# Kernel tuning notes

Hardware: AMD Instinct MI355X
Metric: run time of the kernel (lower is better)

## Reference

```python
import jax, jax.numpy as jnp
import numpy as np

V, H, L, NH, DH, FF, P, T = 21128, 768, 12, 12, 64, 3072, 512, 9
B, S = 16, 256
EPS = 1e-12

def _ln(x, g, b):
    m = x.mean(-1, keepdims=True)
    v = ((x - m) ** 2).mean(-1, keepdims=True)
    return (x - m) * jax.lax.rsqrt(v + EPS) * g + b

def setup_inputs() -> dict:
    key = jax.random.key(0)
    ks = iter(jax.random.split(key, 64))
    def nrm(shape, s=0.02):
        return (jax.random.normal(next(ks), shape, jnp.float32) * s)
    inp = {
        'input_ids': jax.random.randint(next(ks), (B, 1, S), 0, V, dtype=jnp.int32),
        'token_type_ids': jnp.zeros((B, 1, S), jnp.int32),
        'attention_mask': jnp.ones((B, 1, S), jnp.int32),
        'tags': jax.random.randint(next(ks), (B, S), 0, T, dtype=jnp.int32),
        'word_emb': nrm((V, H)), 'pos_emb': nrm((P, H)), 'type_emb': nrm((2, H)),
        'emb_ln_g': jnp.ones((H,), jnp.float32), 'emb_ln_b': jnp.zeros((H,), jnp.float32),
        'Wq': nrm((L, H, H)), 'bq': jnp.zeros((L, H), jnp.float32),
        'Wk': nrm((L, H, H)), 'bk': jnp.zeros((L, H), jnp.float32),
        'Wv': nrm((L, H, H)), 'bv': jnp.zeros((L, H), jnp.float32),
        'Wo': nrm((L, H, H)), 'bo': jnp.zeros((L, H), jnp.float32),
        'ln1_g': jnp.ones((L, H), jnp.float32), 'ln1_b': jnp.zeros((L, H), jnp.float32),
        'W1': nrm((L, H, FF)), 'b1': jnp.zeros((L, FF), jnp.float32),
        'W2': nrm((L, FF, H)), 'b2': jnp.zeros((L, H), jnp.float32),
        'ln2_g': jnp.ones((L, H), jnp.float32), 'ln2_b': jnp.zeros((L, H), jnp.float32),
        'dense_W': nrm((H, T)), 'dense_b': jnp.zeros((T,), jnp.float32),
        'crf_start': nrm((T,), 0.1), 'crf_end': nrm((T,), 0.1), 'crf_trans': nrm((T, T), 0.1),
    }
    return inp

def _model(input_ids, token_type_ids, attention_mask, tags,
           word_emb, pos_emb, type_emb, emb_ln_g, emb_ln_b,
           Wq, bq, Wk, bk, Wv, bv, Wo, bo, ln1_g, ln1_b,
           W1, b1, W2, b2, ln2_g, ln2_b, dense_W, dense_b,
           crf_start, crf_end, crf_trans):
    ids = input_ids[:, 0, :]            # [B,S]
    tt = token_type_ids[:, 0, :]
    amask = attention_mask[:, 0, :]     # [B,S] int
    Bn, Sn = ids.shape
    # --- BERT embeddings (post-LN BERT-base) ---
    x = word_emb[ids] + pos_emb[:Sn][None, :, :] + type_emb[tt]
    x = _ln(x, emb_ln_g, emb_ln_b)
    bias = jnp.where(amask[:, None, None, :] > 0, 0.0, -1e9).astype(x.dtype)  # [B,1,1,S]
    scale = 1.0 / np.sqrt(DH).astype(np.float32)
    def layer(h, p):
        wq, bq_, wk, bk_, wv, bv_, wo, bo_, g1, c1, w1, d1, w2, d2, g2, c2 = p
        q = (h @ wq + bq_).reshape(Bn, Sn, NH, DH).transpose(0, 2, 1, 3)
        k = (h @ wk + bk_).reshape(Bn, Sn, NH, DH).transpose(0, 2, 1, 3)
        v = (h @ wv + bv_).reshape(Bn, Sn, NH, DH).transpose(0, 2, 1, 3)
        att = jax.nn.softmax(jnp.einsum('bhqd,bhkd->bhqk', q, k) * scale + bias, axis=-1)
        ctx = jnp.einsum('bhqk,bhkd->bhqd', att, v).transpose(0, 2, 1, 3).reshape(Bn, Sn, H)
        h = _ln(h + ctx @ wo + bo_, g1, c1)
        ff = jax.nn.gelu(h @ w1 + d1, approximate=False)
        h = _ln(h + ff @ w2 + d2, g2, c2)
        return h, None
    x, _ = jax.lax.scan(layer, x, (Wq, bq, Wk, bk, Wv, bv, Wo, bo, ln1_g, ln1_b, W1, b1, W2, b2, ln2_g, ln2_b))
    # --- emission head, seq-first like the torch code ---
    emis = (x @ dense_W + dense_b).transpose(1, 0, 2)   # [S,B,T]
    m = (amask.T > 0)                                    # [S,B] bool
    tags_sb = tags.T                                     # [S,B]
    bidx = jnp.arange(Bn)
    # --- CRF numerator (gold path score) ---
    score0 = crf_start[tags_sb[0]] + emis[0, bidx, tags_sb[0]]
    def num_step(sc, inp):
        e, t, tp, mm = inp
        inc = crf_trans[tp, t] + e[bidx, t]
        return sc + jnp.where(mm, inc, 0.0), None
    score, _ = jax.lax.scan(num_step, score0, (emis[1:], tags_sb[1:], tags_sb[:-1], m[1:]))
    lengths = m.astype(jnp.int32).sum(0)                 # [B]
    last_tag = jnp.take_along_axis(tags_sb, (lengths - 1)[None, :], axis=0)[0]
    score = score + crf_end[last_tag]
    # --- CRF partition (forward algorithm) ---
    alpha0 = crf_start[None, :] + emis[0]                # [B,T]
    def fwd_step(a, inp):
        e, mm = inp
        nxt = jax.nn.logsumexp(a[:, :, None] + crf_trans[None, :, :] + e[:, None, :], axis=1)
        return jnp.where(mm[:, None], nxt, a), None
    alpha, _ = jax.lax.scan(fwd_step, alpha0, (emis[1:], m[1:]))
    logZ = jax.nn.logsumexp(alpha + crf_end[None, :], axis=-1)
    loss = -(score - logZ).mean()                        # reduction='mean'
    # --- Viterbi decode ---
    v0 = crf_start[None, :] + emis[0]
    tid = jnp.arange(T)
    def vit_step(vv, inp):
        e, mm = inp
        sc = vv[:, :, None] + crf_trans[None, :, :]       # [B,T,T]
        nv = sc.max(1) + e
        idx = sc.argmax(1).astype(jnp.int32)
        vv2 = jnp.where(mm[:, None], nv, vv)
        idx = jnp.where(mm[:, None], idx, tid[None, :].astype(jnp.int32))
        return vv2, idx
    vfin, hist = jax.lax.scan(vit_step, v0, (emis[1:], m[1:]))  # hist: [S-1,B,T]
    last = jnp.argmax(vfin + crf_end[None, :], axis=-1).astype(jnp.int32)  # [B]
    def back_step(t, h):
        prev = jnp.take_along_axis(h, t[:, None], axis=1)[:, 0]
        return prev, prev
    _, path = jax.lax.scan(back_step, last, hist, reverse=True)  # [S-1,B]
    preds = jnp.concatenate([path, last[None, :]], axis=0).T     # [B,S]
    return loss, preds

def reference(input_ids, token_type_ids, attention_mask, tags,
              word_emb, pos_emb, type_emb, emb_ln_g, emb_ln_b,
              Wq, bq, Wk, bk, Wv, bv, Wo, bo, ln1_g, ln1_b,
              W1, b1, W2, b2, ln2_g, ln2_b, dense_W, dense_b,
              crf_start, crf_end, crf_trans):
    return _model(input_ids, token_type_ids, attention_mask, tags,
                  word_emb, pos_emb, type_emb, emb_ln_g, emb_ln_b,
                  Wq, bq, Wk, bk, Wv, bv, Wo, bo, ln1_g, ln1_b,
                  W1, b1, W2, b2, ln2_g, ln2_b, dense_W, dense_b,
                  crf_start, crf_end, crf_trans)
```

## Files before the change

### kernel.cpp

```cpp
#include <hip/hip_runtime.h>
#include <math.h>

#define B_ 16
#define S_ 256
#define H_ 768
#define L_ 12
#define NH_ 12
#define DH_ 64
#define FF_ 3072
#define T_ 9

typedef unsigned short ushort_t;
typedef __attribute__((ext_vector_type(8))) __bf16 bf16x8;
typedef __attribute__((ext_vector_type(4))) float f32x4;
typedef __attribute__((ext_vector_type(4))) unsigned short us4;
typedef __attribute__((ext_vector_type(4))) unsigned int u32x4;

__device__ __forceinline__ ushort_t f2bf(float f) {
  union { float f; unsigned u; } v; v.f = f;
  unsigned r = v.u + 0x7FFFu + ((v.u >> 16) & 1u);
  return (ushort_t)(r >> 16);
}
__device__ __forceinline__ float bf2f(ushort_t h) {
  union { unsigned u; float f; } v; v.u = ((unsigned)h) << 16;
  return v.f;
}
__device__ __forceinline__ void gload16(const void* g, void* l) {
  __builtin_amdgcn_global_load_lds((const __attribute__((address_space(1))) void*)g,
                                   (__attribute__((address_space(3))) void*)l, 16, 0, 0);
}

__global__ __launch_bounds__(256) void emb_ln_kernel(const int* __restrict__ ids, const int* __restrict__ tt,
                              const float* __restrict__ we, const float* __restrict__ pe,
                              const float* __restrict__ te, const float* __restrict__ g,
                              const float* __restrict__ bb, float* __restrict__ out,
                              ushort_t* __restrict__ oh, ushort_t* __restrict__ ol) {
  const int token = blockIdx.x;
  const int tid = threadIdx.x;
  const int s = token & (S_ - 1);
  const int id = ids[token];
  const int t2 = tt[token];
  float x[3];
  float sum = 0.f;
#pragma unroll
  for (int i = 0; i < 3; ++i) {
    int d = tid + i * 256;
    x[i] = we[(size_t)id * H_ + d] + pe[(size_t)s * H_ + d] + te[(size_t)t2 * H_ + d];
    sum += x[i];
  }
  __shared__ float red[4];
#pragma unroll
  for (int o = 32; o > 0; o >>= 1) sum += __shfl_xor(sum, o, 64);
  const int wid = tid >> 6, lane = tid & 63;
  if (lane == 0) red[wid] = sum;
  __syncthreads();
  const float mean = (red[0] + red[1] + red[2] + red[3]) * (1.f / H_);
  float vs = 0.f;
#pragma unroll
  for (int i = 0; i < 3; ++i) { float dv = x[i] - mean; vs += dv * dv; }
#pragma unroll
  for (int o = 32; o > 0; o >>= 1) vs += __shfl_xor(vs, o, 64);
  __syncthreads();
  if (lane == 0) red[wid] = vs;
  __syncthreads();
  const float var = (red[0] + red[1] + red[2] + red[3]) * (1.f / H_);
  const float inv = rsqrtf(var + 1e-12f);
  float* op = out + (size_t)token * H_;
  ushort_t* hp = oh + (size_t)token * H_;
  ushort_t* lp = ol + (size_t)token * H_;
#pragma unroll
  for (int i = 0; i < 3; ++i) {
    int d = tid + i * 256;
    float y = (x[i] - mean) * inv * g[d] + bb[d];
    op[d] = y;
    ushort_t h = f2bf(y);
    hp[d] = h;
    lp[d] = f2bf(y - bf2f(h));
  }
}

__global__ __launch_bounds__(256) void ln_kernel(const float* __restrict__ base, const float* __restrict__ delta,
                          const float* __restrict__ g, const float* __restrict__ bb,
                          float* __restrict__ out, ushort_t* __restrict__ oh, ushort_t* __restrict__ ol) {
  const int token = blockIdx.x;
  const int tid = threadIdx.x;
  const float* bp = base + (size_t)token * H_;
  const float* dp = delta + (size_t)token * H_;
  float x[3];
  float s = 0.f;
#pragma unroll
  for (int i = 0; i < 3; ++i) { int d = tid + i * 256; x[i] = bp[d] + dp[d]; s += x[i]; }
  __shared__ float red[4];
#pragma unroll
  for (int o = 32; o > 0; o >>= 1) s += __shfl_xor(s, o, 64);
  const int wid = tid >> 6, lane = tid & 63;
  if (lane == 0) red[wid] = s;
  __syncthreads();
  const float mean = (red[0] + red[1] + red[2] + red[3]) * (1.f / H_);
  float vs = 0.f;
#pragma unroll
  for (int i = 0; i < 3; ++i) { float dv = x[i] - mean; vs += dv * dv; }
#pragma unroll
  for (int o = 32; o > 0; o >>= 1) vs += __shfl_xor(vs, o, 64);
  __syncthreads();
  if (lane == 0) red[wid] = vs;
  __syncthreads();
  const float var = (red[0] + red[1] + red[2] + red[3]) * (1.f / H_);
  const float inv = rsqrtf(var + 1e-12f);
  float* op = out + (size_t)token * H_;
  ushort_t* hp = oh + (size_t)token * H_;
  ushort_t* lp = ol + (size_t)token * H_;
#pragma unroll
  for (int i = 0; i < 3; ++i) {
    int d = tid + i * 256;
    float y = (x[i] - mean) * inv * g[d] + bb[d];
    op[d] = y;
    ushort_t h = f2bf(y);
    hp[d] = h;
    lp[d] = f2bf(y - bf2f(h));
  }
}

__device__ __forceinline__ void transpose_core(float (*t)[65], const float* __restrict__ src,
                                               ushort_t* __restrict__ dh,
                                               int K, int N, int n0, int k0) {
  const int tid = threadIdx.x;
#pragma unroll
  for (int i = 0; i < 16; ++i) {
    int lin = tid + i * 256;
    int kk = lin >> 6, nn = lin & 63;
    t[kk][nn] = src[(size_t)(k0 + kk) * N + n0 + nn];
  }
  __syncthreads();
#pragma unroll
  for (int i = 0; i < 16; ++i) {
    int lin = tid + i * 256;
    int nn = lin >> 6, kk = lin & 63;
    dh[(size_t)(n0 + nn) * K + k0 + kk] = f2bf(t[kk][nn]);
  }
}

__device__ __forceinline__ void wprep_dispatch(float (*t)[65], int wid,
                        const float* Wq, const float* Wk, const float* Wv, const float* Wo,
                        const float* W1, const float* W2,
                        ushort_t* WT4h, ushort_t* W1th, ushort_t* W2th) {
  if (wid < 576) {
    const int z = wid / 144, r = wid - z * 144;
    const int x = r % 12, y = r / 12;
    const float* src = z == 0 ? Wq : (z == 1 ? Wk : (z == 2 ? Wv : Wo));
    transpose_core(t, src, WT4h + (size_t)z * H_ * H_, H_, H_, x * 64, y * 64);
  } else if (wid < 1152) {
    const int i = wid - 576;
    const int x = i % 48, y = i / 48;
    transpose_core(t, W1, W1th, H_, FF_, x * 64, y * 64);
  } else {
    const int i = wid - 1152;
    const int x = i % 12, y = i / 12;
    transpose_core(t, W2, W2th, FF_, H_, x * 64, y * 64);
  }
}

__global__ __launch_bounds__(256) void wprep_k(const float* __restrict__ Wq, const float* __restrict__ Wk,
                        const float* __restrict__ Wv, const float* __restrict__ Wo,
                        const float* __restrict__ W1, const float* __restrict__ W2,
                        ushort_t* __restrict__ WT4h,
                        ushort_t* __restrict__ W1th, ushort_t* __restrict__ W2th) {
  __shared__ float t[64][65];
  wprep_dispatch(t, blockIdx.x, Wq, Wk, Wv, Wo, W1, W2, WT4h, W1th, W2th);
}

template <int R>
__device__ __forceinline__ void stage_slice(const ushort_t* __restrict__ gsrc, int K, char* lds) {
  const int tid = threadIdx.x;
  constexpr int NIT = (R * 4) / 256;
#pragma unroll
  for (int i = 0; i < NIT; ++i) {
    const int v = tid + i * 256;
    const int kh = v / (2 * R);
    const int r2 = v & (2 * R - 1);
    const int row = r2 >> 1;
    const int kg = (kh << 1) | ((r2 & 1) ^ ((row >> 2) & 1));
    gload16(gsrc + (size_t)row * K + kg * 8, lds + (i * 256 + (tid & 192)) * 16);
  }
}

template <int BM, int BN, int BK>
__device__ __forceinline__ void mgemm_acc(
    const ushort_t* __restrict__ Ah, const ushort_t* __restrict__ Al,
    const ushort_t* __restrict__ Bth,
    int K, f32x4 (&acc)[BM / 32][BN / 32], char* pool) {
  constexpr int FM = BM / 32;
  constexpr int FN = BN / 32;
  constexpr int ABYTES = BM * BK * 2;
  constexpr int BBYTES = BN * BK * 2;
  constexpr int BUF = 2 * ABYTES + BBYTES;
  const int tid = threadIdx.x;
  const int w = tid >> 6, lane = tid & 63;
  const int wm = w >> 1, wn = w & 1;
  const int kgL = lane >> 4, lr = lane & 15;
  const int row0 = blockIdx.y * BM, col0 = blockIdx.x * BN;

#pragma unroll
  for (int i = 0; i < FM; ++i)
#pragma unroll
    for (int j = 0; j < FN; ++j) acc[i][j] = (f32x4){0.f, 0.f, 0.f, 0.f};

  const int khL = kgL >> 1;
  const int swz = (((kgL & 1) ^ ((lr >> 2) & 1)) << 4);
  const int aB0 = khL * (BM * 32) + (wm * (BM / 2) + lr) * 32 + swz;
  const int bB0 = khL * (BN * 32) + (wn * (BN / 2) + lr) * 32 + swz;

  const ushort_t* gA_h = Ah + (size_t)row0 * K;
  const ushort_t* gA_l = Al + (size_t)row0 * K;
  const ushort_t* gB_h = Bth + (size_t)col0 * K;

  auto stageall = [&](int k0, char* buf) {
#pragma unroll
    for (int c = 0; c < BK / 32; ++c) {
      stage_slice<BM>(gA_h + k0 + c * 32, K, buf + c * BM * 64);
      stage_slice<BM>(gA_l + k0 + c * 32, K, buf + ABYTES + c * BM * 64);
      stage_slice<BN>(gB_h + k0 + c * 32, K, buf + 2 * ABYTES + c * BN * 64);
    }
  };

  const int nk = K / BK;
  stageall(0, pool);
  for (int k = 0; k < nk; ++k) {
    char* cur = pool + (k & 1) * BUF;
    if (k + 1 < nk) {
      stageall((k + 1) * BK, pool + ((k + 1) & 1) * BUF);
      asm volatile("s_waitcnt vmcnt(6)" ::: "memory");
    } else {
      asm volatile("s_waitcnt vmcnt(0)" ::: "memory");
    }
    __builtin_amdgcn_s_barrier();
    asm volatile("" ::: "memory");

#pragma unroll
    for (int ks = 0; ks < BK / 32; ++ks) {
      const char* aP = cur + ks * BM * 64;
      const char* bP = cur + 2 * ABYTES + ks * BN * 64;
      bf16x8 a_h[FM], a_l[FM], b_h[FN];
#pragma unroll
      for (int fm = 0; fm < FM; ++fm) {
        a_h[fm] = *(const bf16x8*)(aP + aB0 + fm * 512);
        a_l[fm] = *(const bf16x8*)(aP + ABYTES + aB0 + fm * 512);
      }
#pragma unroll
      for (int fn = 0; fn < FN; ++fn) {
        b_h[fn] = *(const bf16x8*)(bP + bB0 + fn * 512);
      }
#pragma unroll
      for (int fm = 0; fm < FM; ++fm)
#pragma unroll
        for (int fn = 0; fn < FN; ++fn) {
          f32x4 c = acc[fm][fn];
          c = __builtin_amdgcn_mfma_f32_16x16x32_bf16(a_h[fm], b_h[fn], c, 0, 0, 0);
          c = __builtin_amdgcn_mfma_f32_16x16x32_bf16(a_l[fm], b_h[fn], c, 0, 0, 0);
          acc[fm][fn] = c;
        }
    }
    asm volatile("" ::: "memory");
    __builtin_amdgcn_s_barrier();
  }
}

template <int BM, int BN, int BK, int EPI>
__global__ __launch_bounds__(256, 3) void mgemm(const ushort_t* __restrict__ Ah, const ushort_t* __restrict__ Al,
                      const ushort_t* __restrict__ Bth,
                      const float* __restrict__ bias, float* __restrict__ Cf,
                      ushort_t* __restrict__ Ch, ushort_t* __restrict__ Cl, int N, int K) {
  __shared__ __attribute__((aligned(16))) char pool[2 * (2 * BM * BK + BN * BK) * 2];
  f32x4 acc[BM / 32][BN / 32];
  mgemm_acc<BM, BN, BK>(Ah, Al, Bth, K, acc, pool);
  const int tid = threadIdx.x;
  const int w = tid >> 6, lane = tid & 63;
  const int wm = w >> 1, wn = w & 1;
  const int kg = lane >> 4, lr = lane & 15;
  const int row0 = blockIdx.y * BM, col0 = blockIdx.x * BN;
#pragma unroll
  for (int fn = 0; fn < BN / 32; ++fn) {
    const int col = col0 + wn * (BN / 2) + fn * 16 + lr;
    const float bv = bias[col];
#pragma unroll
    for (int fm = 0; fm < BM / 32; ++fm) {
#pragma unroll
      for (int r = 0; r < 4; ++r) {
        const int row = row0 + wm * (BM / 2) + fm * 16 + kg * 4 + r;
        float v = acc[fm][fn][r] + bv;
        if (EPI == 0) {
          Cf[(size_t)row * N + col] = v;
        } else {
          float gl = 0.5f * v * (1.f + erff(v * 0.70710678118654752f));
          ushort_t h = f2bf(gl);
          Ch[(size_t)row * N + col] = h;
          Cl[(size_t)row * N + col] = f2bf(gl - bf2f(h));
        }
      }
    }
  }
}

__global__ __launch_bounds__(256, 3) void ff1_fused(
    const ushort_t* __restrict__ Xh, const ushort_t* __restrict__ Xl,
    const ushort_t* __restrict__ W1th, const float* __restrict__ bias,
    ushort_t* __restrict__ Ch, ushort_t* __restrict__ Cl,
    const float* __restrict__ WqN, const float* __restrict__ WkN,
    const float* __restrict__ WvN, const float* __restrict__ WoN,
    const float* __restrict__ W1N, const float* __restrict__ W2N,
    ushort_t* __restrict__ WT4hN, ushort_t* __restrict__ W1thN, ushort_t* __restrict__ W2thN) {
  __shared__ __attribute__((aligned(16))) char pool[49152];
  if (blockIdx.y >= 32) {
    if (WqN == nullptr) return;
    const int wid = (blockIdx.y - 32) * 24 + blockIdx.x;
    wprep_dispatch((float(*)[65])pool, wid, WqN, WkN, WvN, WoN, W1N, W2N, WT4hN, W1thN, W2thN);
    return;
  }
  f32x4 acc[4][4];
  mgemm_acc<128, 128, 32>(Xh, Xl, W1th, H_, acc, pool);
  const int tid = threadIdx.x;
  const int w = tid >> 6, lane = tid & 63;
  const int wm = w >> 1, wn = w & 1;
  const int kg = lane >> 4, lr = lane & 15;
  const int row0 = blockIdx.y * 128, col0 = blockIdx.x * 128;
#pragma unroll
  for (int fn = 0; fn < 4; ++fn) {
    const int col = col0 + wn * 64 + fn * 16 + lr;
    const float bv = bias[col];
#pragma unroll
    for (int fm = 0; fm < 4; ++fm) {
#pragma unroll
      for (int r = 0; r < 4; ++r) {
        const int row = row0 + wm * 64 + fm * 16 + kg * 4 + r;
        float v = acc[fm][fn][r] + bv;
        float gl = 0.5f * v * (1.f + erff(v * 0.70710678118654752f));
        ushort_t h = f2bf(gl);
        Ch[(size_t)row * FF_ + col] = h;
        Cl[(size_t)row * FF_ + col] = f2bf(gl - bf2f(h));
      }
    }
  }
}

__global__ __launch_bounds__(256) void qkv_m(const ushort_t* __restrict__ Xh, const ushort_t* __restrict__ Xl,
                      const ushort_t* __restrict__ WT4h,
                      const float* __restrict__ bq, const float* __restrict__ bk,
                      const float* __restrict__ bvv,
                      ushort_t* __restrict__ Qh, ushort_t* __restrict__ Ql,
                      ushort_t* __restrict__ Kh, ushort_t* __restrict__ Vth) {
  constexpr int ABYTES = 128 * 32 * 2;
  constexpr int BUF = 2 * ABYTES + 3 * ABYTES;
  __shared__ __attribute__((aligned(16))) char pool[2 * BUF];
  const int tid = threadIdx.x;
  const int w = tid >> 6, lane = tid & 63;
  const int wm = w >> 1, wn = w & 1;
  const int kgL = lane >> 4, lr = lane & 15;
  const int row0 = blockIdx.y * 128, col0 = blockIdx.x * 128;

  f32x4 acc[3][4][4];
#pragma unroll
  for (int z = 0; z < 3; ++z)
#pragma unroll
    for (int i = 0; i < 4; ++i)
#pragma unroll
      for (int j = 0; j < 4; ++j) acc[z][i][j] = (f32x4){0.f, 0.f, 0.f, 0.f};

  const int khL = kgL >> 1;
  const int swz = (((kgL & 1) ^ ((lr >> 2) & 1)) << 4);
  const int aB0 = khL * (128 * 32) + (wm * 64 + lr) * 32 + swz;
  const int bB0 = khL * (128 * 32) + (wn * 64 + lr) * 32 + swz;

  const ushort_t* gA_h = Xh + (size_t)row0 * H_;
  const ushort_t* gA_l = Xl + (size_t)row0 * H_;
  const ushort_t* gB0 = WT4h + (size_t)col0 * H_;
  const ushort_t* gB1 = WT4h + (size_t)H_ * H_ + (size_t)col0 * H_;
  const ushort_t* gB2 = WT4h + (size_t)2 * H_ * H_ + (size_t)col0 * H_;

  auto stageall = [&](int k0, char* buf) {
    stage_slice<128>(gA_h + k0, H_, buf);
    stage_slice<128>(gA_l + k0, H_, buf + ABYTES);
    stage_slice<128>(gB0 + k0, H_, buf + 2 * ABYTES);
    stage_slice<128>(gB1 + k0, H_, buf + 3 * ABYTES);
    stage_slice<128>(gB2 + k0, H_, buf + 4 * ABYTES);
  };

  const int nk = H_ / 32;
  stageall(0, pool);
  for (int k = 0; k < nk; ++k) {
    char* cur = pool + (k & 1) * BUF;
    if (k + 1 < nk) {
      stageall((k + 1) * 32, pool + ((k + 1) & 1) * BUF);
      asm volatile("s_waitcnt vmcnt(10)" ::: "memory");
    } else {
      asm volatile("s_waitcnt vmcnt(0)" ::: "memory");
    }
    __builtin_amdgcn_s_barrier();
    asm volatile("" ::: "memory");

    bf16x8 a_h[4], a_l[4];
#pragma unroll
    for (int fm = 0; fm < 4; ++fm) {
      a_h[fm] = *(const bf16x8*)(cur + aB0 + fm * 512);
      a_l[fm] = *(const bf16x8*)(cur + ABYTES + aB0 + fm * 512);
    }
#pragma unroll
    for (int z = 0; z < 3; ++z) {
      const char* bP = cur + (2 + z) * ABYTES;
      bf16x8 b_h[4];
#pragma unroll
      for (int fn = 0; fn < 4; ++fn) b_h[fn] = *(const bf16x8*)(bP + bB0 + fn * 512);
#pragma unroll
      for (int fm = 0; fm < 4; ++fm)
#pragma unroll
        for (int fn = 0; fn < 4; ++fn) {
          f32x4 c = acc[z][fm][fn];
          c = __builtin_amdgcn_mfma_f32_16x16x32_bf16(a_h[fm], b_h[fn], c, 0, 0, 0);
          c = __builtin_amdgcn_mfma_f32_16x16x32_bf16(a_l[fm], b_h[fn], c, 0, 0, 0);
          acc[z][fm][fn] = c;
        }
    }
    asm volatile("" ::: "memory");
    __builtin_amdgcn_s_barrier();
  }

  const int kg = kgL;
#pragma unroll
  for (int fn = 0; fn < 4; ++fn) {
    const int col = col0 + wn * 64 + fn * 16 + lr;
    const float bvq = bq[col], bvk = bk[col], bvv2 = bvv[col];
#pragma unroll
    for (int fm = 0; fm < 4; ++fm) {
      const int rowb = row0 + wm * 64 + fm * 16 + kg * 4;
#pragma unroll
      for (int r = 0; r < 4; ++r) {
        float v = acc[0][fm][fn][r] + bvq;
        ushort_t h = f2bf(v);
        Qh[(size_t)(rowb + r) * H_ + col] = h;
        Ql[(size_t)(rowb + r) * H_ + col] = f2bf(v - bf2f(h));
      }
#pragma unroll
      for (int r = 0; r < 4; ++r) {
        Kh[(size_t)(rowb + r) * H_ + col] = f2bf(acc[1][fm][fn][r] + bvk);
      }
      {
        us4 h4;
#pragma unroll
        for (int r = 0; r < 4; ++r) h4[r] = f2bf(acc[2][fm][fn][r] + bvv2);
        const int bb2 = rowb >> 8, s0 = rowb & 255;
        const int hh2 = col >> 6, d = col & 63;
        *(us4*)(Vth + ((size_t)(bb2 * NH_ + hh2) * DH_ + d) * S_ + s0) = h4;
      }
    }
  }
}

__global__ __launch_bounds__(256, 3) void attn_mfma(
    const ushort_t* __restrict__ Qh, const ushort_t* __restrict__ Ql,
    const ushort_t* __restrict__ Kh, const ushort_t* __restrict__ Vth,
    const int* __restrict__ amask,
    ushort_t* __restrict__ Oh, ushort_t* __restrict__ Ol) {
  const int bid = blockIdx.x;
  const int qt = bid / 192;
  const int gh = bid - qt * 192;
  const int b = gh / NH_;
  const int h = gh - b * NH_;
  __shared__ __attribute__((aligned(16))) ushort_t sKh[2][64 * 64];
  __shared__ __attribute__((aligned(16))) ushort_t sVh[2][64 * 64];
  __shared__ __attribute__((aligned(16))) unsigned sP[4][16 * 68];
  __shared__ float sBias[2][64];
  const int tid = threadIdx.x;
  const int w = tid >> 6, lane = tid & 63;
  const int kg = lane >> 4, lr = lane & 15;

  const int qrow = b * S_ + qt * 64 + w * 16 + lr;
  bf16x8 qfh[2], qfl[2];
#pragma unroll
  for (int ds2 = 0; ds2 < 2; ++ds2) {
    const size_t off = (size_t)qrow * H_ + h * DH_ + ds2 * 32 + kg * 8;
    qfh[ds2] = *(const bf16x8*)(Qh + off);
    qfl[ds2] = *(const bf16x8*)(Ql + off);
  }

  f32x4 ctx[4];
#pragma unroll
  for (int i = 0; i < 4; ++i) ctx[i] = (f32x4){0.f, 0.f, 0.f, 0.f};
  float mrow[4], lrw[4];
#pragma unroll
  for (int r = 0; r < 4; ++r) { mrow[r] = -1e30f; lrw[r] = 0.f; }

  unsigned* sPw = &sP[w][0];

  auto stageKV = [&](int kt, int bufi) {
#pragma unroll
    for (int i = 0; i < 2; ++i) {
      const int v = tid + i * 256;
      const int row = v >> 3;
      const int c16 = (v & 7) ^ (row & 7);
      const size_t kgl = (size_t)(b * S_ + kt * 64 + row) * H_ + h * DH_ + c16 * 8;
      gload16(Kh + kgl, (char*)&sKh[bufi][0] + v * 16);
      const size_t vgl = (size_t)((b * NH_ + h) * DH_ + row) * S_ + kt * 64 + c16 * 8;
      gload16(Vth + vgl, (char*)&sVh[bufi][0] + v * 16);
    }
    if (tid < 64) sBias[bufi][tid] = (amask[b * S_ + kt * 64 + tid] > 0) ? 0.f : -1e9f;
  };

  stageKV(0, 0);
  for (int kt = 0; kt < 4; ++kt) {
    const int bi = kt & 1;
    if (kt < 3) {
      stageKV(kt + 1, bi ^ 1);
      asm volatile("s_waitcnt vmcnt(4) lgkmcnt(0)" ::: "memory");
    } else {
      asm volatile("s_waitcnt vmcnt(0) lgkmcnt(0)" ::: "memory");
    }
    __builtin_amdgcn_s_barrier();
    asm volatile("" ::: "memory");

    f32x4 sc[4];
#pragma unroll
    for (int kf = 0; kf < 4; ++kf) sc[kf] = (f32x4){0.f, 0.f, 0.f, 0.f};
#pragma unroll
    for (int kf = 0; kf < 4; ++kf) {
      const int krow = kf * 16 + lr;
#pragma unroll
      for (int ds2 = 0; ds2 < 2; ++ds2) {
        const int cb = (ds2 * 64 + kg * 16) ^ ((krow & 7) << 4);
        const bf16x8 kvh = *(const bf16x8*)((const char*)&sKh[bi][0] + krow * 128 + cb);
        sc[kf] = __builtin_amdgcn_mfma_f32_16x16x32_bf16(qfh[ds2], kvh, sc[kf], 0, 0, 0);
        sc[kf] = __builtin_amdgcn_mfma_f32_16x16x32_bf16(qfl[ds2], kvh, sc[kf], 0, 0, 0);
      }
    }
    float bsv[4];
#pragma unroll
    for (int kf = 0; kf < 4; ++kf) bsv[kf] = sBias[bi][kf * 16 + lr];

#pragma unroll
    for (int r = 0; r < 4; ++r) {
      float sv[4];
      float tmax = -1e30f;
#pragma unroll
      for (int kf = 0; kf < 4; ++kf) {
        sv[kf] = sc[kf][r] * 0.125f + bsv[kf];
        tmax = fmaxf(tmax, sv[kf]);
      }
#pragma unroll
      for (int o = 8; o > 0; o >>= 1) tmax = fmaxf(tmax, __shfl_xor(tmax, o, 64));
      const float mnew = fmaxf(mrow[r], tmax);
      const float corr = expf(mrow[r] - mnew);
      float ls = 0.f;
      const int qoff = (kg * 4 + r) * 68;
#pragma unroll
      for (int kf = 0; kf < 4; ++kf) {
        const float pe = expf(sv[kf] - mnew);
        ls += pe;
        const ushort_t hi = f2bf(pe);
        const ushort_t lo = f2bf(pe - bf2f(hi));
        sPw[qoff + kf * 16 + lr] = ((unsigned)hi << 16) | lo;
      }
#pragma unroll
      for (int o = 8; o > 0; o >>= 1) ls += __shfl_xor(ls, o, 64);
      lrw[r] = lrw[r] * corr + ls;
      mrow[r] = mnew;
#pragma unroll
      for (int df = 0; df < 4; ++df) ctx[df][r] *= corr;
    }

#pragma unroll
    for (int ks = 0; ks < 2; ++ks) {
      unsigned w8[8];
      *(u32x4*)&w8[0] = *(const u32x4*)(sPw + lr * 68 + ks * 32 + kg * 8);
      *(u32x4*)&w8[4] = *(const u32x4*)(sPw + lr * 68 + ks * 32 + kg * 8 + 4);
      union { bf16x8 v; ushort_t u[8]; } ph, pl;
#pragma unroll
      for (int j = 0; j < 8; ++j) { ph.u[j] = (ushort_t)(w8[j] >> 16); pl.u[j] = (ushort_t)(w8[j] & 0xffffu); }
#pragma unroll
      for (int df = 0; df < 4; ++df) {
        const int vrow = df * 16 + lr;
        const int cb = (ks * 64 + kg * 16) ^ ((vrow & 7) << 4);
        const bf16x8 vvh = *(const bf16x8*)((const char*)&sVh[bi][0] + vrow * 128 + cb);
        ctx[df] = __builtin_amdgcn_mfma_f32_16x16x32_bf16(ph.v, vvh, ctx[df], 0, 0, 0);
        ctx[df] = __builtin_amdgcn_mfma_f32_16x16x32_bf16(pl.v, vvh, ctx[df], 0, 0, 0);
      }
    }
    asm volatile("" ::: "memory");
    __builtin_amdgcn_s_barrier();
  }

#pragma unroll
  for (int r = 0; r < 4; ++r) {
    const float inv = 1.f / lrw[r];
    const int tok = b * S_ + qt * 64 + w * 16 + kg * 4 + r;
#pragma unroll
    for (int df = 0; df < 4; ++df) {
      const float v = ctx[df][r] * inv;
      const ushort_t hi = f2bf(v);
      const size_t o = (size_t)tok * H_ + h * DH_ + df * 16 + lr;
      Oh[o] = hi;
      Ol[o] = f2bf(v - bf2f(hi));
    }
  }
}

__global__ __launch_bounds__(256) void emis_kernel(const float* __restrict__ X, const float* __restrict__ W,
                            const float* __restrict__ bias, float* __restrict__ E) {
  const int wave = (blockIdx.x * 256 + threadIdx.x) >> 6;
  const int lane = threadIdx.x & 63;
  const int b = wave >> 8, s = wave & 255;
  const float* xp = X + (size_t)wave * H_;
  float acc[T_];
#pragma unroll
  for (int t = 0; t < T_; ++t) acc[t] = 0.f;
  for (int i = 0; i < 12; ++i) {
    const int d = lane + i * 64;
    const float xv = xp[d];
    const float* wp = W + (size_t)d * T_;
#pragma unroll
    for (int t = 0; t < T_; ++t) acc[t] = fmaf(xv, wp[t], acc[t]);
  }
#pragma unroll
  for (int t = 0; t < T_; ++t) {
    float v = acc[t];
#pragma unroll
    for (int o = 32; o > 0; o >>= 1) v += __shfl_xor(v, o, 64);
    acc[t] = v;
  }
  if (lane < T_) E[((size_t)s * B_ + b) * T_ + lane] = acc[lane] + bias[lane];
}

__global__ __launch_bounds__(128) void crf_kernel(const float* __restrict__ emis, const int* __restrict__ tags,
                          const int* __restrict__ amask,
                          const float* __restrict__ crf_start, const float* __restrict__ crf_end,
                          const float* __restrict__ trans,
                          float* __restrict__ partial, float* __restrict__ out) {
  const int b = blockIdx.x;
  const int tid = threadIdx.x;
  const int wv = tid >> 6;
  const int lane = tid & 63;
  __shared__ float sE[S_ * T_];
  __shared__ float sM[S_];
  __shared__ float trs[T_ * T_];
  __shared__ unsigned char hist[S_ - 1][16];
  __shared__ float pathf[S_];
  for (int i = tid; i < S_ * T_; i += 128) {
    const int s = i / T_, t = i - s * T_;
    sE[i] = emis[((size_t)s * B_ + b) * T_ + t];
  }
  for (int i = tid; i < S_; i += 128) sM[i] = (float)amask[b * S_ + i];
  for (int i = tid; i < T_ * T_; i += 128) trs[i] = trans[i];
  __syncthreads();

  const int t = lane;
  const bool act = t < T_;
  float trc[T_];
#pragma unroll
  for (int p = 0; p < T_; ++p) trc[p] = act ? trs[p * T_ + t] : 0.f;

  if (wv == 0) {
    float alpha = act ? crf_start[t] + sE[t] : 0.f;
    for (int s = 1; s < S_; ++s) {
      float ap[T_];
#pragma unroll
      for (int p = 0; p < T_; ++p) ap[p] = __shfl(alpha, p, 64);
      if (act) {
        const float e = sE[s * T_ + t];
        float mx = -1e30f;
#pragma unroll
        for (int p = 0; p < T_; ++p) mx = fmaxf(mx, ap[p] + trc[p]);
        float sum = 0.f;
#pragma unroll
        for (int p = 0; p < T_; ++p) sum += __expf(ap[p] + trc[p] - mx);
        const float na = mx + __logf(sum) + e;
        if (sM[s] > 0.f) alpha = na;
      }
    }
    float nsum = 0.f;
    int len = 0;
#pragma unroll
    for (int j = 0; j < 4; ++j) {
      const int s = lane + j * 64;
      const int mk = (sM[s] > 0.f) ? 1 : 0;
      len += mk;
      if (s >= 1 && mk) {
        const int tc = tags[b * S_ + s], tp = tags[b * S_ + s - 1];
        nsum += trs[tp * T_ + tc] + sE[s * T_ + tc];
      }
    }
#pragma unroll
    for (int o = 32; o > 0; o >>= 1) {
      nsum += __shfl_xor(nsum, o, 64);
      len += __shfl_xor(len, o, 64);
    }
    const float fz = act ? alpha + crf_end[t] : -1e30f;
    float zp[T_];
#pragma unroll
    for (int p = 0; p < T_; ++p) zp[p] = __shfl(fz, p, 64);
    if (lane == 0) {
      float mx = -1e30f;
#pragma unroll
      for (int p = 0; p < T_; ++p) mx = fmaxf(mx, zp[p]);
      float sum = 0.f;
#pragma unroll
      for (int p = 0; p < T_; ++p) sum += __expf(zp[p] - mx);
      const float logZ = mx + __logf(sum);
      const int tg0 = tags[b * S_];
      const float score = nsum + crf_start[tg0] + sE[tg0] + crf_end[tags[b * S_ + len - 1]];
      partial[b] = score - logZ;
    }
  } else {
    float vit = act ? crf_start[t] + sE[t] : 0.f;
    for (int s = 1; s < S_; ++s) {
      float vp[T_];
#pragma unroll
      for (int p = 0; p < T_; ++p) vp[p] = __shfl(vit, p, 64);
      if (act) {
        const float e = sE[s * T_ + t];
        float best = -1e30f; int bi = 0;
#pragma unroll
        for (int p = 0; p < T_; ++p) {
          const float scv = vp[p] + trc[p];
          if (scv > best) { best = scv; bi = p; }
        }
        if (sM[s] > 0.f) {
          vit = best + e;
          hist[s - 1][t] = (unsigned char)bi;
        } else {
          hist[s - 1][t] = (unsigned char)t;
        }
      }
    }
    const float fv = act ? vit + crf_end[t] : -1e30f;
    float wp[T_];
#pragma unroll
    for (int p = 0; p < T_; ++p) wp[p] = __shfl(fv, p, 64);
    if (lane == 0) {
      float best = -1e30f; int lastTag = 0;
#pragma unroll
      for (int p = 0; p < T_; ++p) {
        if (wp[p] > best) { best = wp[p]; lastTag = p; }
      }
      int tc = lastTag;
      pathf[S_ - 1] = (float)tc;
      for (int i = S_ - 2; i >= 0; --i) {
        tc = hist[i][tc];
        pathf[i] = (float)tc;
      }
    }
  }
  __syncthreads();
#pragma unroll
  for (int j = 0; j < 2; ++j) {
    const int s = tid + j * 128;
    out[1 + b * S_ + s] = pathf[s];
  }
}

__global__ __launch_bounds__(64) void crf_final(const float* __restrict__ partial, float* __restrict__ out) {
  const int lane = threadIdx.x;
  float v = (lane < B_) ? partial[lane] : 0.f;
#pragma unroll
  for (int o = 32; o > 0; o >>= 1) v += __shfl_xor(v, o, 64);
  if (lane == 0) out[0] = -(v * (1.f / B_));
}

extern "C" void kernel_launch(void* const* d_in, const int* in_sizes, int n_in,
                              void* d_out, int out_size, void* d_ws, size_t ws_size,
                              hipStream_t stream) {
  const int* input_ids = (const int*)d_in[0];
  const int* token_type_ids = (const int*)d_in[1];
  const int* attention_mask = (const int*)d_in[2];
  const int* tags = (const int*)d_in[3];
  const float* word_emb = (const float*)d_in[4];
  const float* pos_emb = (const float*)d_in[5];
  const float* type_emb = (const float*)d_in[6];
  const float* emb_ln_g = (const float*)d_in[7];
  const float* emb_ln_b = (const float*)d_in[8];
  const float* Wq = (const float*)d_in[9];
  const float* bq = (const float*)d_in[10];
  const float* Wk = (const float*)d_in[11];
  const float* bk = (const float*)d_in[12];
  const float* Wv = (const float*)d_in[13];
  const float* bv = (const float*)d_in[14];
  const float* Wo = (const float*)d_in[15];
  const float* bo = (const float*)d_in[16];
  const float* ln1_g = (const float*)d_in[17];
  const float* ln1_b = (const float*)d_in[18];
  const float* W1 = (const float*)d_in[19];
  const float* b1 = (const float*)d_in[20];
  const float* W2 = (const float*)d_in[21];
  const float* b2 = (const float*)d_in[22];
  const float* ln2_g = (const float*)d_in[23];
  const float* ln2_b = (const float*)d_in[24];
  const float* dense_W = (const float*)d_in[25];
  const float* dense_b = (const float*)d_in[26];
  const float* crf_start = (const float*)d_in[27];
  const float* crf_end = (const float*)d_in[28];
  const float* crf_trans = (const float*)d_in[29];

  constexpr size_t NTOK = (size_t)B_ * S_;
  constexpr size_t XSZ = NTOK * H_;
  constexpr size_t WT4SZ = (size_t)4 * H_ * H_;
  constexpr size_t WFSZ = (size_t)H_ * FF_;

  char* p = (char*)d_ws;
  float* X = (float*)p;            p += XSZ * 4;
  float* TMP = (float*)p;          p += XSZ * 4;
  char* UN = p;                    p += 8 * XSZ * 2;
  ushort_t* Qh = (ushort_t*)UN;
  ushort_t* Ql = Qh + XSZ;
  ushort_t* Kh = Ql + XSZ;
  ushort_t* Vth = Kh + XSZ;
  ushort_t* CTXh = Vth + XSZ;
  ushort_t* CTXl = CTXh + XSZ;
  ushort_t* FFh = (ushort_t*)UN;
  ushort_t* FFl = FFh + NTOK * FF_;
  ushort_t* Xh = (ushort_t*)p;     p += XSZ * 2;
  ushort_t* Xl = (ushort_t*)p;     p += XSZ * 2;
  ushort_t* WT4h2 = (ushort_t*)p;  p += WT4SZ * 2 * 2;
  ushort_t* W1th2 = (ushort_t*)p;  p += WFSZ * 2 * 2;
  ushort_t* W2th2 = (ushort_t*)p;  p += WFSZ * 2 * 2;
  float* EM = (float*)p;           p += (size_t)S_ * B_ * T_ * 4;
  float* PART = (float*)p;         p += B_ * 4;

  emb_ln_kernel<<<dim3(4096), dim3(256), 0, stream>>>(input_ids, token_type_ids, word_emb, pos_emb,
                                                      type_emb, emb_ln_g, emb_ln_b, X, Xh, Xl);
  wprep_k<<<dim3(1728), dim3(256), 0, stream>>>(Wq, Wk, Wv, Wo, W1, W2, WT4h2, W1th2, W2th2);

  for (int l = 0; l < L_; ++l) {
    const int pr = l & 1, pn = (l + 1) & 1;
    ushort_t* WT4h = WT4h2 + (size_t)pr * WT4SZ;
    ushort_t* W1th = W1th2 + (size_t)pr * WFSZ;
    ushort_t* W2th = W2th2 + (size_t)pr * WFSZ;
    const bool hasNext = (l + 1 < L_);
    const size_t wo_n = (size_t)(l + 1) * H_ * H_;

    qkv_m<<<dim3(6, 32), dim3(256), 0, stream>>>(Xh, Xl, WT4h, bq + (size_t)l * H_,
                                                 bk + (size_t)l * H_, bv + (size_t)l * H_,
                                                 Qh, Ql, Kh, Vth);
    attn_mfma<<<dim3(768), dim3(256), 0, stream>>>(Qh, Ql, Kh, Vth, attention_mask, CTXh, CTXl);
    mgemm<128, 128, 32, 0><<<dim3(6, 32), dim3(256), 0, stream>>>(
        CTXh, CTXl, WT4h + (size_t)3 * H_ * H_,
        bo + (size_t)l * H_, TMP, nullptr, nullptr, H_, H_);
    ln_kernel<<<dim3(4096), dim3(256), 0, stream>>>(X, TMP, ln1_g + (size_t)l * H_,
                                                    ln1_b + (size_t)l * H_, X, Xh, Xl);
    ff1_fused<<<dim3(24, 32 + 72), dim3(256), 0, stream>>>(
        Xh, Xl, W1th, b1 + (size_t)l * FF_, FFh, FFl,
        hasNext ? Wq + wo_n : nullptr, Wk + wo_n, Wv + wo_n, Wo + wo_n,
        W1 + (size_t)(l + 1) * WFSZ, W2 + (size_t)(l + 1) * WFSZ,
        WT4h2 + (size_t)pn * WT4SZ, W1th2 + (size_t)pn * WFSZ, W2th2 + (size_t)pn * WFSZ);
    mgemm<128, 128, 32, 0><<<dim3(6, 32), dim3(256), 0, stream>>>(
        FFh, FFl, W2th, b2 + (size_t)l * H_, TMP, nullptr, nullptr, H_, FF_);
    ln_kernel<<<dim3(4096), dim3(256), 0, stream>>>(X, TMP, ln2_g + (size_t)l * H_,
                                                    ln2_b + (size_t)l * H_, X, Xh, Xl);
  }

  emis_kernel<<<dim3(1024), dim3(256), 0, stream>>>(X, dense_W, dense_b, EM);
  crf_kernel<<<dim3(B_), dim3(128), 0, stream>>>(EM, tags, attention_mask, crf_start, crf_end,
                                                 crf_trans, PART, (float*)d_out);
  crf_final<<<dim3(1), dim3(64), 0, stream>>>(PART, (float*)d_out);
}
```

Baseline: 3.163 ms.

## Widen FF1 tile to 128x256, fuse final LN with emissions, LDS broadcast in CRF

The FF1 GEMM now uses 128x256 tiles with a larger LDS pool and lower occupancy (launch bounds 2). The grid is halved in x, the weight-prep block count is doubled to keep the same coverage, and the vmcnt wait is made tile-dependent. The last layer's LayerNorm is fused with the 9-tag emission projection, which drops a kernel launch and a full read of X. The CRF forward and Viterbi loops broadcast per-tag values through LDS instead of nine shuffles. The wider tile gives more reuse but means fewer blocks and more register pressure.

```diff
diff --git a/kernel.cpp b/kernel.cpp
--- a/kernel.cpp
+++ b/kernel.cpp
@@ -118,6 +118,67 @@
     ushort_t h = f2bf(y);
     hp[d] = h;
     lp[d] = f2bf(y - bf2f(h));
+  }
+}
+
+__global__ __launch_bounds__(256) void ln_emis_kernel(const float* __restrict__ base, const float* __restrict__ delta,
+                               const float* __restrict__ g, const float* __restrict__ bb,
+                               const float* __restrict__ W, const float* __restrict__ wbias,
+                               float* __restrict__ E) {
+  const int token = blockIdx.x;
+  const int tid = threadIdx.x;
+  __shared__ float sW[H_ * T_];
+  __shared__ float red[4];
+  __shared__ float wred[4][12];
+  for (int i = tid; i < H_ * T_; i += 256) sW[i] = W[i];
+
+  const float* bp = base + (size_t)token * H_;
+  const float* dp = delta + (size_t)token * H_;
+  float x[3];
+  float s = 0.f;
+#pragma unroll
+  for (int i = 0; i < 3; ++i) { int d = tid + i * 256; x[i] = bp[d] + dp[d]; s += x[i]; }
+#pragma unroll
+  for (int o = 32; o > 0; o >>= 1) s += __shfl_xor(s, o, 64);
+  const int wid = tid >> 6, lane = tid & 63;
+  if (lane == 0) red[wid] = s;
+  __syncthreads();
+  const float mean = (red[0] + red[1] + red[2] + red[3]) * (1.f / H_);
+  float vs = 0.f;
+#pragma unroll
+  for (int i = 0; i < 3; ++i) { float dv = x[i] - mean; vs += dv * dv; }
+#pragma unroll
+  for (int o = 32; o > 0; o >>= 1) vs += __shfl_xor(vs, o, 64);
+  __syncthreads();
+  if (lane == 0) red[wid] = vs;
+  __syncthreads();
+  const float var = (red[0] + red[1] + red[2] + red[3]) * (1.f / H_);
+  const float inv = rsqrtf(var + 1e-12f);
+
+  float acc9[T_];
+#pragma unroll
+  for (int t = 0; t < T_; ++t) acc9[t] = 0.f;
+#pragma unroll
+  for (int i = 0; i < 3; ++i) {
+    int d = tid + i * 256;
+    float y = (x[i] - mean) * inv * g[d] + bb[d];
+    const float* wr = sW + d * T_;
+#pragma unroll
+    for (int t = 0; t < T_; ++t) acc9[t] = fmaf(y, wr[t], acc9[t]);
+  }
+#pragma unroll
+  for (int o = 32; o > 0; o >>= 1)
+#pragma unroll
+    for (int t = 0; t < T_; ++t) acc9[t] += __shfl_xor(acc9[t], o, 64);
+  if (lane == 0) {
+#pragma unroll
+    for (int t = 0; t < T_; ++t) wred[wid][t] = acc9[t];
+  }
+  __syncthreads();
+  if (tid < T_) {
+    const float v = wred[0][tid] + wred[1][tid] + wred[2][tid] + wred[3][tid] + wbias[tid];
+    const int b2 = token >> 8, s2 = token & 255;
+    E[((size_t)s2 * B_ + b2) * T_ + tid] = v;
   }
 }
 
@@ -194,6 +255,7 @@
   constexpr int ABYTES = BM * BK * 2;
   constexpr int BBYTES = BN * BK * 2;
   constexpr int BUF = 2 * ABYTES + BBYTES;
+  constexpr int NL = (8 * BM + 4 * BN) / 256;
   const int tid = threadIdx.x;
   const int w = tid >> 6, lane = tid & 63;
   const int wm = w >> 1, wn = w & 1;
@@ -229,7 +291,13 @@
     char* cur = pool + (k & 1) * BUF;
     if (k + 1 < nk) {
       stageall((k + 1) * BK, pool + ((k + 1) & 1) * BUF);
-      asm volatile("s_waitcnt vmcnt(6)" ::: "memory");
+      if constexpr (NL == 6) {
+        asm volatile("s_waitcnt vmcnt(6)" ::: "memory");
+      } else if constexpr (NL == 8) {
+        asm volatile("s_waitcnt vmcnt(8)" ::: "memory");
+      } else {
+        asm volatile("s_waitcnt vmcnt(0)" ::: "memory");
+      }
     } else {
       asm volatile("s_waitcnt vmcnt(0)" ::: "memory");
     }
@@ -301,7 +369,7 @@
   }
 }
 
-__global__ __launch_bounds__(256, 3) void ff1_fused(
+__global__ __launch_bounds__(256, 2) void ff1_fused(
     const ushort_t* __restrict__ Xh, const ushort_t* __restrict__ Xl,
     const ushort_t* __restrict__ W1th, const float* __restrict__ bias,
     ushort_t* __restrict__ Ch, ushort_t* __restrict__ Cl,
@@ -309,23 +377,23 @@
     const float* __restrict__ WvN, const float* __restrict__ WoN,
     const float* __restrict__ W1N, const float* __restrict__ W2N,
     ushort_t* __restrict__ WT4hN, ushort_t* __restrict__ W1thN, ushort_t* __restrict__ W2thN) {
-  __shared__ __attribute__((aligned(16))) char pool[49152];
+  __shared__ __attribute__((aligned(16))) char pool[2 * (2 * 128 * 32 + 256 * 32) * 2];
   if (blockIdx.y >= 32) {
     if (WqN == nullptr) return;
-    const int wid = (blockIdx.y - 32) * 24 + blockIdx.x;
+    const int wid = (blockIdx.y - 32) * 12 + blockIdx.x;
     wprep_dispatch((float(*)[65])pool, wid, WqN, WkN, WvN, WoN, W1N, W2N, WT4hN, W1thN, W2thN);
     return;
   }
-  f32x4 acc[4][4];
-  mgemm_acc<128, 128, 32>(Xh, Xl, W1th, H_, acc, pool);
+  f32x4 acc[4][8];
+  mgemm_acc<128, 256, 32>(Xh, Xl, W1th, H_, acc, pool);
   const int tid = threadIdx.x;
   const int w = tid >> 6, lane = tid & 63;
   const int wm = w >> 1, wn = w & 1;
   const int kg = lane >> 4, lr = lane & 15;
-  const int row0 = blockIdx.y * 128, col0 = blockIdx.x * 128;
-#pragma unroll
-  for (int fn = 0; fn < 4; ++fn) {
-    const int col = col0 + wn * 64 + fn * 16 + lr;
+  const int row0 = blockIdx.y * 128, col0 = blockIdx.x * 256;
+#pragma unroll
+  for (int fn = 0; fn < 8; ++fn) {
+    const int col = col0 + wn * 128 + fn * 16 + lr;
     const float bv = bias[col];
 #pragma unroll
     for (int fm = 0; fm < 4; ++fm) {
@@ -601,32 +669,6 @@
   }
 }
 
-__global__ __launch_bounds__(256) void emis_kernel(const float* __restrict__ X, const float* __restrict__ W,
-                            const float* __restrict__ bias, float* __restrict__ E) {
-  const int wave = (blockIdx.x * 256 + threadIdx.x) >> 6;
-  const int lane = threadIdx.x & 63;
-  const int b = wave >> 8, s = wave & 255;
-  const float* xp = X + (size_t)wave * H_;
-  float acc[T_];
-#pragma unroll
-  for (int t = 0; t < T_; ++t) acc[t] = 0.f;
-  for (int i = 0; i < 12; ++i) {
-    const int d = lane + i * 64;
-    const float xv = xp[d];
-    const float* wp = W + (size_t)d * T_;
-#pragma unroll
-    for (int t = 0; t < T_; ++t) acc[t] = fmaf(xv, wp[t], acc[t]);
-  }
-#pragma unroll
-  for (int t = 0; t < T_; ++t) {
-    float v = acc[t];
-#pragma unroll
-    for (int o = 32; o > 0; o >>= 1) v += __shfl_xor(v, o, 64);
-    acc[t] = v;
-  }
-  if (lane < T_) E[((size_t)s * B_ + b) * T_ + lane] = acc[lane] + bias[lane];
-}
-
 __global__ __launch_bounds__(128) void crf_kernel(const float* __restrict__ emis, const int* __restrict__ tags,
                           const int* __restrict__ amask,
                           const float* __restrict__ crf_start, const float* __restrict__ crf_end,
@@ -641,6 +683,7 @@
   __shared__ float trs[T_ * T_];
   __shared__ unsigned char hist[S_ - 1][16];
   __shared__ float pathf[S_];
+  __shared__ __attribute__((aligned(16))) float sBr[2][16];
   for (int i = tid; i < S_ * T_; i += 128) {
     const int s = i / T_, t = i - s * T_;
     sE[i] = emis[((size_t)s * B_ + b) * T_ + t];
@@ -658,17 +701,23 @@
   if (wv == 0) {
     float alpha = act ? crf_start[t] + sE[t] : 0.f;
     for (int s = 1; s < S_; ++s) {
-      float ap[T_];
-#pragma unroll
-      for (int p = 0; p < T_; ++p) ap[p] = __shfl(alpha, p, 64);
+      if (act) sBr[0][t] = alpha;
+      asm volatile("s_waitcnt lgkmcnt(0)" ::: "memory");
+      float ap[12];
+      *(f32x4*)&ap[0] = *(const f32x4*)&sBr[0][0];
+      *(f32x4*)&ap[4] = *(const f32x4*)&sBr[0][4];
+      ap[8] = sBr[0][8];
       if (act) {
         const float e = sE[s * T_ + t];
-        float mx = -1e30f;
-#pragma unroll
-        for (int p = 0; p < T_; ++p) mx = fmaxf(mx, ap[p] + trc[p]);
+        float v[T_];
+#pragma unroll
+        for (int p = 0; p < T_; ++p) v[p] = ap[p] + trc[p];
+        float m0 = fmaxf(fmaxf(v[0], v[1]), fmaxf(v[2], v[3]));
+        float m1 = fmaxf(fmaxf(v[4], v[5]), fmaxf(v[6], v[7]));
+        const float mx = fmaxf(fmaxf(m0, m1), v[8]);
         float sum = 0.f;
 #pragma unroll
-        for (int p = 0; p < T_; ++p) sum += __expf(ap[p] + trc[p] - mx);
+        for (int p = 0; p < T_; ++p) sum += __expf(v[p] - mx);
         const float na = mx + __logf(sum) + e;
         if (sM[s] > 0.f) alpha = na;
       }
@@ -690,11 +739,12 @@
       nsum += __shfl_xor(nsum, o, 64);
       len += __shfl_xor(len, o, 64);
     }
-    const float fz = act ? alpha + crf_end[t] : -1e30f;
-    float zp[T_];
-#pragma unroll
-    for (int p = 0; p < T_; ++p) zp[p] = __shfl(fz, p, 64);
+    if (act) sBr[0][t] = alpha + crf_end[t];
+    asm volatile("s_waitcnt lgkmcnt(0)" ::: "memory");
     if (lane == 0) {
+      float zp[T_];
+#pragma unroll
+      for (int p = 0; p < T_; ++p) zp[p] = sBr[0][p];
       float mx = -1e30f;
 #pragma unroll
       for (int p = 0; p < T_; ++p) mx = fmaxf(mx, zp[p]);
@@ -709,9 +759,12 @@
   } else {
     float vit = act ? crf_start[t] + sE[t] : 0.f;
     for (int s = 1; s < S_; ++s) {
-      float vp[T_];
-#pragma unroll
-      for (int p = 0; p < T_; ++p) vp[p] = __shfl(vit, p, 64);
+      if (act) sBr[1][t] = vit;
+      asm volatile("s_waitcnt lgkmcnt(0)" ::: "memory");
+      float vp[12];
+      *(f32x4*)&vp[0] = *(const f32x4*)&sBr[1][0];
+      *(f32x4*)&vp[4] = *(const f32x4*)&sBr[1][4];
+      vp[8] = sBr[1][8];
       if (act) {
         const float e = sE[s * T_ + t];
         float best = -1e30f; int bi = 0;
@@ -728,15 +781,14 @@
         }
       }
     }
-    const float fv = act ? vit + crf_end[t] : -1e30f;
-    float wp[T_];
-#pragma unroll
-    for (int p = 0; p < T_; ++p) wp[p] = __shfl(fv, p, 64);
+    if (act) sBr[1][t] = vit + crf_end[t];
+    asm volatile("s_waitcnt lgkmcnt(0)" ::: "memory");
     if (lane == 0) {
       float best = -1e30f; int lastTag = 0;
 #pragma unroll
       for (int p = 0; p < T_; ++p) {
-        if (wp[p] > best) { best = wp[p]; lastTag = p; }
+        const float wpv = sBr[1][p];
+        if (wpv > best) { best = wpv; lastTag = p; }
       }
       int tc = lastTag;
       pathf[S_ - 1] = (float)tc;
@@ -842,18 +894,23 @@
         bo + (size_t)l * H_, TMP, nullptr, nullptr, H_, H_);
     ln_kernel<<<dim3(4096), dim3(256), 0, stream>>>(X, TMP, ln1_g + (size_t)l * H_,
                                                     ln1_b + (size_t)l * H_, X, Xh, Xl);
-    ff1_fused<<<dim3(24, 32 + 72), dim3(256), 0, stream>>>(
+    ff1_fused<<<dim3(12, 32 + 144), dim3(256), 0, stream>>>(
         Xh, Xl, W1th, b1 + (size_t)l * FF_, FFh, FFl,
         hasNext ? Wq + wo_n : nullptr, Wk + wo_n, Wv + wo_n, Wo + wo_n,
         W1 + (size_t)(l + 1) * WFSZ, W2 + (size_t)(l + 1) * WFSZ,
         WT4h2 + (size_t)pn * WT4SZ, W1th2 + (size_t)pn * WFSZ, W2th2 + (size_t)pn * WFSZ);
     mgemm<128, 128, 32, 0><<<dim3(6, 32), dim3(256), 0, stream>>>(
         FFh, FFl, W2th, b2 + (size_t)l * H_, TMP, nullptr, nullptr, H_, FF_);
-    ln_kernel<<<dim3(4096), dim3(256), 0, stream>>>(X, TMP, ln2_g + (size_t)l * H_,
-                                                    ln2_b + (size_t)l * H_, X, Xh, Xl);
-  }
-
-  emis_kernel<<<dim3(1024), dim3(256), 0, stream>>>(X, dense_W, dense_b, EM);
+    if (l + 1 < L_) {
+      ln_kernel<<<dim3(4096), dim3(256), 0, stream>>>(X, TMP, ln2_g + (size_t)l * H_,
+                                                      ln2_b + (size_t)l * H_, X, Xh, Xl);
+    } else {
+      ln_emis_kernel<<<dim3(4096), dim3(256), 0, stream>>>(X, TMP, ln2_g + (size_t)l * H_,
+                                                           ln2_b + (size_t)l * H_, dense_W,
+                                                           dense_b, EM);
+    }
+  }
+
   crf_kernel<<<dim3(B_), dim3(128), 0, stream>>>(EM, tags, attention_mask, crf_start, crf_end,
                                                  crf_trans, PART, (float*)d_out);
   crf_final<<<dim3(1), dim3(64), 0, stream>>>(PART, (float*)d_out);
```

New measurement: 3.164 ms. No clear change (+0.0%).
